# Kernel optimization log

Measured on AMD Instinct MI355X. Metric: run time of the kernel, lower is better.

Reference implementation:

```python
import jax, jax.numpy as jnp
import numpy as np

CUTOFF = 4          # lattice cutoff radius (module init arg)
NMAX = 64           # padded max neighbors per mobile site (~58 actual at cutoff=4)
BATCH = 131072      # number of independent configurations
B_SOFT = 0.01       # softening constant b in vint
FAR = 1e6           # padding position, masked out


def _rot(c):
    return np.array([[np.cos(c), -np.sin(c)], [np.sin(c), np.cos(c)]])


def _build_geometry():
    """Replicates PotEnergy1P.__init__ (with the intended, bug-fixed math)."""
    s3 = np.sqrt(3.0)
    base = [np.array([0.5, s3 / 6]), np.array([1.0, -s3 / 3]),
            np.array([1.5, s3 / 6]), np.array([1.0, 2 * s3 / 3])]
    mobile = base \
        + [_rot(2 * np.pi / 3) @ p for p in base] \
        + [_rot(4 * np.pi / 3) @ p for p in base]
    mobile = np.stack(mobile)                      # [12, 2]

    def ntopos(n1, n2):
        return np.array([0.5, s3 / 6]) + n1 * np.array([1.0, 0.0]) \
            + n2 * np.array([-0.5, s3 / 2])

    rng = range(-4 * CUTOFF, 4 * CUTOFF)
    grid = np.array([ntopos(n1, n2) for n1 in rng for n2 in rng])  # [G, 2]
    dist = np.linalg.norm(grid[:, None, :] - mobile[None, :, :], axis=-1)  # [G, 12]
    not_mobile = ~np.any(np.isclose(dist, 0.0, atol=1e-8), axis=1)        # [G]

    neighbors = np.full((12, NMAX, 2), FAR, dtype=np.float32)
    mask = np.zeros((12, NMAX), dtype=np.float32)
    for i in range(12):
        idx = np.where(not_mobile & (dist[:, i] < CUTOFF))[0]
        k = len(idx)
        assert k <= NMAX
        neighbors[i, :k] = grid[idx]
        mask[i, :k] = 1.0
    return neighbors, mask


def setup_inputs() -> dict:
    key = jax.random.key(0)
    x = jax.random.normal(key, (BATCH, 24), dtype=jnp.float32)
    neighbors, mask = _build_geometry()
    return {"x": x,
            "neighbors": jnp.asarray(neighbors),
            "mask": jnp.asarray(mask)}


def reference(x, neighbors, mask):
    # x: [B, 24] -> [B, 12, 2] mobile positions
    xr = x.reshape(x.shape[0], -1, 2)
    # pairwise displacement to all padded neighbors: [B, 12, NMAX, 2]
    d = xr[:, :, None, :] - neighbors[None, :, :, :]
    r = jnp.sqrt(jnp.sum(d * d, axis=-1))          # [B, 12, NMAX]
    v = jnp.exp(-r) / (r + B_SOFT)                 # vint with a=1.0, b=0.01
    return jnp.sum(v * mask[None], axis=(1, 2))    # [B] total potential energy
```

## Files before the change

### kernel.cpp

```cpp
#include <hip/hip_runtime.h>

#define NMAX   64
#define NSITES 12
#define SPLIT  4
#define BLOCK  256
#define ROWS   66

#define LOG2E  1.44269504088896340736f
#define LN2    0.69314718055994530942f
#define B_SOFT 0.01f
#define PAD_C  2.0e6f

__global__ __launch_bounds__(BLOCK, 8)
void pot_energy_kernel(const float* __restrict__ x,
                       const float* __restrict__ neighbors,
                       const float* __restrict__ mask,
                       float* __restrict__ out, int B) {
    __shared__ float2 nb[NSITES * ROWS];
    __shared__ int    cnt[NSITES];

    const int tid  = threadIdx.x;
    const int wv   = tid >> 6;
    const int lane = tid & 63;

    for (int idx = tid; idx < NSITES * ROWS; idx += BLOCK)
        nb[idx] = make_float2(PAD_C, PAD_C);
    __syncthreads();

    for (int s = wv; s < NSITES; s += 4) {
        const bool keep = mask[s * NMAX + lane] > 0.5f;
        const unsigned long long bal = __ballot(keep);
        if (keep) {
            const int pos = __popcll(bal & ((1ull << lane) - 1ull));
            const float2 p = ((const float2*)neighbors)[s * NMAX + lane];
            nb[s * ROWS + pos] = make_float2(p.x * LOG2E, p.y * LOG2E);
        }
        if (lane == 0) cnt[s] = __popcll(bal);
    }
    __syncthreads();

    int m = 0;
    #pragma unroll
    for (int s = 0; s < NSITES; ++s) m = max(m, cnt[s]);
    m = __builtin_amdgcn_readfirstlane(m);

    const int gtid = blockIdx.x * BLOCK + tid;
    const int e = gtid >> 2;
    const int q = gtid & 3;
    if (e >= B) return;

    const float2* xp = (const float2*)(x + (size_t)gtid * 6);
    const float2 p0 = xp[0], p1 = xp[1], p2 = xp[2];
    const float xs_[3] = { p0.x * LOG2E, p1.x * LOG2E, p2.x * LOG2E };
    const float ys_[3] = { p0.y * LOG2E, p1.y * LOG2E, p2.y * LOG2E };

    float acc = 0.f;
    #pragma unroll
    for (int s = 0; s < 3; ++s) {
        const int site = q * 3 + s;
        const float xs = xs_[s];
        const float ys = ys_[s];
        const float2* __restrict__ row = &nb[site * ROWS];
        #pragma unroll 8
        for (int j = 0; j < m; ++j) {
            const float2 nj = row[j];
            const float dx = xs - nj.x;
            const float dy = ys - nj.y;
            const float r2 = fmaf(dy, dy, dx * dx);
            const float rp = __builtin_amdgcn_sqrtf(r2);
            const float ex = __builtin_amdgcn_exp2f(-rp);
            const float dn = fmaf(rp, LN2, B_SOFT);
            acc = fmaf(ex, __builtin_amdgcn_rcpf(dn), acc);
        }
    }

    acc += __shfl_xor(acc, 1);
    acc += __shfl_xor(acc, 2);
    if (q == 0) out[e] = acc;
}

extern "C" void kernel_launch(void* const* d_in, const int* in_sizes, int n_in,
                              void* d_out, int out_size, void* d_ws, size_t ws_size,
                              hipStream_t stream) {
    const float* x   = (const float*)d_in[0];
    const float* nbr = (const float*)d_in[1];
    const float* msk = (const float*)d_in[2];
    float* out = (float*)d_out;

    const int B = in_sizes[0] / 24;
    const int total_threads = B * SPLIT;
    const int blocks = (total_threads + BLOCK - 1) / BLOCK;
    pot_energy_kernel<<<blocks, BLOCK, 0, stream>>>(x, nbr, msk, out, B);
}
```

Baseline: 86.76 us.

## Replace exp2 with packed polynomial and batch reciprocals four at a time

```diff
diff --git a/kernel.cpp b/kernel.cpp
--- a/kernel.cpp
+++ b/kernel.cpp
@@ -4,27 +4,38 @@
 #define NSITES 12
 #define SPLIT  4
 #define BLOCK  256
-#define ROWS   66
+#define RS     68
 
 #define LOG2E  1.44269504088896340736f
 #define LN2    0.69314718055994530942f
 #define B_SOFT 0.01f
-#define PAD_C  2.0e6f
+#define PAD_C  4.0e4f
+
+#define A1 0.69314718056f
+#define A2 0.24022650700f
+#define A3 0.05550410866f
+#define A4 0.00961812911f
+
+typedef float v2f __attribute__((ext_vector_type(2)));
 
 __global__ __launch_bounds__(BLOCK, 8)
 void pot_energy_kernel(const float* __restrict__ x,
                        const float* __restrict__ neighbors,
                        const float* __restrict__ mask,
                        float* __restrict__ out, int B) {
-    __shared__ float2 nb[NSITES * ROWS];
-    __shared__ int    cnt[NSITES];
+    __shared__ float nbx[NSITES][RS];
+    __shared__ float nby[NSITES][RS];
+    __shared__ int   cnt[NSITES];
 
     const int tid  = threadIdx.x;
     const int wv   = tid >> 6;
     const int lane = tid & 63;
 
-    for (int idx = tid; idx < NSITES * ROWS; idx += BLOCK)
-        nb[idx] = make_float2(PAD_C, PAD_C);
+    for (int idx = tid; idx < NSITES * RS; idx += BLOCK) {
+        const int s = idx / RS, j = idx - s * RS;
+        nbx[s][j] = PAD_C;
+        nby[s][j] = PAD_C;
+    }
     __syncthreads();
 
     for (int s = wv; s < NSITES; s += 4) {
@@ -33,7 +44,8 @@
         if (keep) {
             const int pos = __popcll(bal & ((1ull << lane) - 1ull));
             const float2 p = ((const float2*)neighbors)[s * NMAX + lane];
-            nb[s * ROWS + pos] = make_float2(p.x * LOG2E, p.y * LOG2E);
+            nbx[s][pos] = p.x * LOG2E;
+            nby[s][pos] = p.y * LOG2E;
         }
         if (lane == 0) cnt[s] = __popcll(bal);
     }
@@ -42,7 +54,7 @@
     int m = 0;
     #pragma unroll
     for (int s = 0; s < NSITES; ++s) m = max(m, cnt[s]);
-    m = __builtin_amdgcn_readfirstlane(m);
+    m = (__builtin_amdgcn_readfirstlane(m) + 3) & ~3;
 
     const int gtid = blockIdx.x * BLOCK + tid;
     const int e = gtid >> 2;
@@ -58,19 +70,55 @@
     #pragma unroll
     for (int s = 0; s < 3; ++s) {
         const int site = q * 3 + s;
-        const float xs = xs_[s];
-        const float ys = ys_[s];
-        const float2* __restrict__ row = &nb[site * ROWS];
-        #pragma unroll 8
-        for (int j = 0; j < m; ++j) {
-            const float2 nj = row[j];
-            const float dx = xs - nj.x;
-            const float dy = ys - nj.y;
-            const float r2 = fmaf(dy, dy, dx * dx);
-            const float rp = __builtin_amdgcn_sqrtf(r2);
-            const float ex = __builtin_amdgcn_exp2f(-rp);
-            const float dn = fmaf(rp, LN2, B_SOFT);
-            acc = fmaf(ex, __builtin_amdgcn_rcpf(dn), acc);
+        const v2f xs2 = { xs_[s], xs_[s] };
+        const v2f ys2 = { ys_[s], ys_[s] };
+        const float* __restrict__ rx = nbx[site];
+        const float* __restrict__ ry = nby[site];
+        for (int j0 = 0; j0 < m; j0 += 4) {
+            const float4 nx4 = *(const float4*)(rx + j0);
+            const float4 ny4 = *(const float4*)(ry + j0);
+            const v2f nxa = { nx4.x, nx4.y }, nxb = { nx4.z, nx4.w };
+            const v2f nya = { ny4.x, ny4.y }, nyb = { ny4.z, ny4.w };
+
+            const v2f dxa = xs2 - nxa, dxb = xs2 - nxb;
+            const v2f dya = ys2 - nya, dyb = ys2 - nyb;
+            const v2f r2a = dya * dya + dxa * dxa;
+            const v2f r2b = dyb * dyb + dxb * dxb;
+
+            v2f rpa, rpb;
+            rpa.x = __builtin_amdgcn_sqrtf(r2a.x);
+            rpa.y = __builtin_amdgcn_sqrtf(r2a.y);
+            rpb.x = __builtin_amdgcn_sqrtf(r2b.x);
+            rpb.y = __builtin_amdgcn_sqrtf(r2b.y);
+
+            const v2f da = rpa * LN2 + B_SOFT;
+            const v2f db = rpb * LN2 + B_SOFT;
+
+            v2f fma_, fmb_;
+            fma_.x = __builtin_rintf(rpa.x);
+            fma_.y = __builtin_rintf(rpa.y);
+            fmb_.x = __builtin_rintf(rpb.x);
+            fmb_.y = __builtin_rintf(rpb.y);
+            const v2f ga = fma_ - rpa;
+            const v2f gb = fmb_ - rpb;
+            v2f ha = ((A4 * ga + A3) * ga + A2) * ga + A1;
+            ha = ha * ga + 1.0f;
+            v2f hb = ((A4 * gb + A3) * gb + A2) * gb + A1;
+            hb = hb * gb + 1.0f;
+            const float ex0 = __builtin_ldexpf(ha.x, (int)(-fma_.x));
+            const float ex1 = __builtin_ldexpf(ha.y, (int)(-fma_.y));
+            const float ex2 = __builtin_ldexpf(hb.x, (int)(-fmb_.x));
+            const float ex3 = __builtin_ldexpf(hb.y, (int)(-fmb_.y));
+
+            const float d0 = da.x, d1 = da.y, d2 = db.x, d3 = db.y;
+            const float p01 = d0 * d1;
+            const float p23 = d2 * d3;
+            const float n01 = fmaf(ex1, d0, ex0 * d1);
+            const float n23 = fmaf(ex3, d2, ex2 * d3);
+            const float den = p01 * p23;
+            const float R   = __builtin_amdgcn_rcpf(den);
+            const float N   = fmaf(n23, p01, n01 * p23);
+            acc = fmaf(N, R, acc);
         }
     }
 
```

New measurement: 92.55 us. +6.7%, slower.
